# Performance work log

Hardware: AMD Instinct MI355X
Metric: run time of the kernel (lower is better)

The kernel has to match this reference:

```python
import jax, jax.numpy as jnp
import numpy as np

B, S, IN_DIM, MEM, LAYERS, HEADS, TOP_K = 64, 256, 512, 256, 3, 8, 200


def setup_inputs() -> dict:
    key = jax.random.key(0)
    ks = jax.random.split(key, 16)
    inputs = jax.random.normal(ks[0], (B, S, IN_DIM), jnp.float32)
    # dependency-style sparse 0/1 adjacency, symmetric with self loops
    a = (jax.random.uniform(ks[1], (B, S, S)) < 0.05).astype(jnp.float32)
    adj = jnp.clip(a + jnp.swapaxes(a, -1, -2) + jnp.eye(S, dtype=jnp.float32), 0.0, 1.0)
    lengths = jnp.maximum(jax.random.randint(ks[2], (B,), 0, S + 1), 32)
    pad = jnp.arange(S)[None, :] >= lengths[:, None]  # [B,S] True at pad positions
    score_mask = pad[:, None, :, None] | pad[:, None, None, :]  # [B,1,S,S]
    d = {"adj": adj, "inputs": inputs, "score_mask": score_mask}

    def lin(k, din, dout):
        k1, k2 = jax.random.split(k)
        s = 1.0 / np.sqrt(din)
        return (jax.random.uniform(k1, (din, dout), jnp.float32, -s, s),
                jax.random.uniform(k2, (dout,), jnp.float32, -s, s))

    ki = 3
    for l in range(LAYERS):
        w, b = lin(ks[ki], IN_DIM + l * MEM, MEM); ki += 1
        d[f"W{l}_w"], d[f"W{l}_b"] = w, b
    for i in range(LAYERS - 1):
        din = IN_DIM + (i + 1) * MEM
        qw, qb = lin(ks[ki], din, din); ki += 1
        kw, kb = lin(ks[ki], din, din); ki += 1
        d[f"attn{i}_qw"], d[f"attn{i}_qb"] = qw, qb
        d[f"attn{i}_kw"], d[f"attn{i}_kb"] = kw, kb
    return d


def _gcn_layer(adj, x, denom, W, b):
    # AxW = W(adj @ x) / denom ; out = relu(AxW) + W(x)   (dropout=identity, eval)
    AxW = ((adj @ x) @ W + b) / denom
    return jax.nn.relu(AxW) + (x @ W + b)


def _mha_adj(x, qw, qb, kw, kb, mask):
    Bn, Sn, D = x.shape
    dk = D // HEADS
    q = (x @ qw + qb).reshape(Bn, Sn, HEADS, dk).transpose(0, 2, 1, 3)
    k = (x @ kw + kb).reshape(Bn, Sn, HEADS, dk).transpose(0, 2, 1, 3)
    scores = jnp.einsum('bhqd,bhkd->bhqk', q, k) / jnp.sqrt(jnp.float32(dk))
    scores = jnp.where(mask, jnp.float32(-1e9), scores)
    keep = (~mask[:, :, :, 0:1]).astype(scores.dtype)  # zero out pad query rows
    return jax.nn.softmax(scores, axis=-1) * keep


def _select(m, top_num):
    # per-batch top-k threshold over flattened [S*S], symmetrize, diag := 1
    Bn, Sn, _ = m.shape
    flat = m.reshape(Bn, -1)
    thr = jax.lax.top_k(flat, top_num)[0][:, -1:]
    sel = (flat >= thr).astype(m.dtype).reshape(Bn, Sn, Sn)
    sel = sel + jnp.swapaxes(sel, -1, -2)
    eye = jnp.eye(Sn, dtype=m.dtype)
    return sel * (1.0 - eye) + eye


def reference(adj, inputs, score_mask, W0_w, W0_b, W1_w, W1_b, W2_w, W2_b,
              attn0_qw, attn0_qb, attn0_kw, attn0_kb,
              attn1_qw, attn1_qb, attn1_kw, attn1_kb):
    Ws = [(W0_w, W0_b), (W1_w, W1_b), (W2_w, W2_b)]
    attns = [(attn0_qw, attn0_qb, attn0_kw, attn0_kb),
             (attn1_qw, attn1_qb, attn1_kw, attn1_kb)]
    denom = adj.sum(2, keepdims=True) + 1.0
    out = _gcn_layer(adj, inputs, denom, *Ws[0])
    x = inputs
    for i in range(1, LAYERS):
        x = jnp.concatenate([x, out], axis=-1)  # growing concatenated features
        a = _mha_adj(x, *attns[i - 1], score_mask)  # [B,H,S,S]
        a = a.sum(axis=1)  # second_layer='sum' branch
        a = _select(a, TOP_K) * a
        denom = a.sum(2, keepdims=True) + 1.0
        out = _gcn_layer(a, x, denom, *Ws[i])
    return out
```

## Files before the change

kernel.cpp:

```cpp
#include <hip/hip_runtime.h>
#include <math.h>


typedef __attribute__((ext_vector_type(8))) short s16x8;
typedef __attribute__((ext_vector_type(4))) float f32x4;

__device__ __forceinline__ short f2bf(float x) {
    unsigned u = __float_as_uint(x);
    u += 0x7FFF + ((u >> 16) & 1);
    return (short)(u >> 16);
}
__device__ __forceinline__ float bf2f(short h) {
    return __uint_as_float(((unsigned)(unsigned short)h) << 16);
}

__device__ __forceinline__ void gl2l(const void* g, void* l) {
    __builtin_amdgcn_global_load_lds(
        (const __attribute__((address_space(1))) unsigned int*)g,
        (__attribute__((address_space(3))) unsigned int*)l, 16, 0, 0);
}

__global__ void init_flags(int* flags) {
    if (threadIdx.x < 3) flags[threadIdx.x] = 0;
}

__global__ void detect_mask(const unsigned int* __restrict__ w, int nwords, int* flags) {
    int stride = gridDim.x * blockDim.x;
    int l_u8 = 0, l_f32 = 0, l_nz = 0;
    for (int i = blockIdx.x * blockDim.x + threadIdx.x; i < nwords; i += stride) {
        unsigned v = w[i];
        if (v) {
            l_nz = 1;
            if (v == 0x3F800000u) l_f32 = 1;
            else if (v > 1u) l_u8 = 1;
        }
    }
    if (__ballot(l_u8) && (threadIdx.x & 63) == 0) atomicOr(&flags[0], 1);
    if (__ballot(l_f32) && (threadIdx.x & 63) == 0) atomicOr(&flags[1], 1);
    if (__ballot(l_nz) && (threadIdx.x & 63) == 0) atomicOr(&flags[2], 1);
}

__global__ void extract_pad(const void* __restrict__ mask, const int* __restrict__ flags,
                            unsigned char* __restrict__ pad) {
    int b = blockIdx.x, i = threadIdx.x;
    int v;
    size_t idx = (size_t)b * 65536 + (size_t)i * 256;
    if (flags[0]) v = ((const unsigned char*)mask)[idx] != 0;
    else if (flags[2]) v = ((const unsigned int*)mask)[idx] != 0;
    else v = 0;
    pad[b * 256 + i] = (unsigned char)v;
}

__global__ void build_live(const unsigned char* __restrict__ pad, int* __restrict__ live) {
    if (threadIdx.x == 0) {
        int c = 0;
        for (int t = 0; t < 128; ++t)
            if (!pad[t * 128]) live[1 + c++] = t;
        live[0] = c;
    }
}

__global__ void split_mat(const float* __restrict__ src, int ldsrc, int width,
                          short* __restrict__ dh, short* __restrict__ dl, int ldd) {
    int row = blockIdx.x;
    for (int c = threadIdx.x; c < width; c += 256) {
        float v = src[(size_t)row * ldsrc + c];
        short h = f2bf(v);
        dh[(size_t)row * ldd + c] = h;
        dl[(size_t)row * ldd + c] = f2bf(v - bf2f(h));
    }
}

__global__ void transpose_split(const float* __restrict__ in,
                                short* __restrict__ outh, short* __restrict__ outl,
                                int R, int C, int HR, long PSTR, int rowoff, int outld) {
    __shared__ float tile[32][33];
    int c0 = blockIdx.x * 32, r0 = blockIdx.y * 32;
    int tx = threadIdx.x & 31, ty = threadIdx.x >> 5;
    for (int rr = ty; rr < 32; rr += 8)
        tile[rr][tx] = in[(size_t)(r0 + rr) * C + c0 + tx];
    __syncthreads();
    for (int rr = ty; rr < 32; rr += 8) {
        float v = tile[tx][rr];
        int orow = c0 + rr;
        size_t o = (size_t)(orow / HR) * PSTR + (size_t)((orow % HR) + rowoff) * outld + (r0 + tx);
        short h = f2bf(v);
        outh[o] = h;
        outl[o] = f2bf(v - bf2f(h));
    }
}

__global__ void pack_bias2(const float* __restrict__ qb, const float* __restrict__ kb,
                           float* __restrict__ dst, int D) {
    int i = blockIdx.x * 256 + threadIdx.x;
    if (i < D) {
        int p = i / (D / 2), r = i % (D / 2);
        dst[(size_t)p * D + r] = qb[i];
        dst[(size_t)p * D + D / 2 + r] = kb[i];
    }
}

__global__ __launch_bounds__(256) void mgemm(
    const short* __restrict__ Ah, const short* __restrict__ Al,
    const short* __restrict__ Bh, const short* __restrict__ Bl,
    const float* __restrict__ bias,
    float* __restrict__ C, short* __restrict__ Ch, short* __restrict__ Cl,
    const unsigned char* __restrict__ padArr, const int* __restrict__ liveArr,
    int K, int lda, int ldb, int ldc, int coloff, int zdiv,
    long sA1, long sA2, long sB1, long sB2, long sC1, long sC2,
    float alpha, int skipmode, int swap) {
    int z = blockIdx.z, zq = z / zdiv, zr = z % zdiv;
    int m0, n0;
    if (swap) { m0 = blockIdx.x * 128; n0 = blockIdx.y * 128; }
    else      { m0 = blockIdx.y * 128; n0 = blockIdx.x * 128; }
    if (skipmode == 2 && (padArr[zr * 256 + m0] || padArr[zr * 256 + n0])) return;
    if (skipmode == 3) {
        int cnt = liveArr[0];
        if ((int)blockIdx.x >= cnt) return;
        m0 = liveArr[1 + blockIdx.x] * 128;
    }
    const short* Ahb = Ah + (size_t)zq * sA1 + (size_t)zr * sA2;
    const short* Alb = Al + (size_t)zq * sA1 + (size_t)zr * sA2;
    const short* Bhb = Bh + (size_t)zq * sB1 + (size_t)zr * sB2;
    const short* Blb = Bl + (size_t)zq * sB1 + (size_t)zr * sB2;
    size_t offC = (size_t)zq * sC1 + (size_t)zr * sC2;
    __shared__ short lds[16384];
    int t = threadIdx.x;
    int lane = t & 63, w = t >> 6;
    int wm = w >> 1, wn = w & 1;
    f32x4 acc[4][4];
#pragma unroll
    for (int i = 0; i < 4; ++i)
#pragma unroll
        for (int j = 0; j < 4; ++j)
            acc[i][j] = (f32x4){0.f, 0.f, 0.f, 0.f};

    for (int k0 = 0; k0 < K; k0 += 32) {
        __syncthreads();
#pragma unroll
        for (int p = 0; p < 2; ++p) {
            int s = t + p * 256;
            int mi = (s >> 6) * 16 + (s & 15);
            int koff = k0 + ((s >> 4) & 3) * 8;
            size_t oa = (size_t)(m0 + mi) * lda + koff;
            size_t ob = (size_t)(n0 + mi) * ldb + koff;
            gl2l(Ahb + oa, &lds[s * 8]);
            gl2l(Alb + oa, &lds[4096 + s * 8]);
            gl2l(Bhb + ob, &lds[8192 + s * 8]);
            gl2l(Blb + ob, &lds[12288 + s * 8]);
        }
        __syncthreads();
        s16x8 ah[4], al4[4], bh[4], bl4[4];
#pragma unroll
        for (int i = 0; i < 4; ++i) {
            int off = ((wm * 4 + i) * 64 + lane) * 8;
            ah[i] = *(const s16x8*)&lds[off];
            al4[i] = *(const s16x8*)&lds[4096 + off];
        }
#pragma unroll
        for (int j = 0; j < 4; ++j) {
            int off = ((wn * 4 + j) * 64 + lane) * 8;
            bh[j] = *(const s16x8*)&lds[8192 + off];
            bl4[j] = *(const s16x8*)&lds[12288 + off];
        }
#pragma unroll
        for (int i = 0; i < 4; ++i)
#pragma unroll
            for (int j = 0; j < 4; ++j) {
                acc[i][j] = __builtin_amdgcn_mfma_f32_16x16x32_bf16(ah[i], bh[j], acc[i][j], 0, 0, 0);
                acc[i][j] = __builtin_amdgcn_mfma_f32_16x16x32_bf16(ah[i], bl4[j], acc[i][j], 0, 0, 0);
                acc[i][j] = __builtin_amdgcn_mfma_f32_16x16x32_bf16(al4[i], bh[j], acc[i][j], 0, 0, 0);
            }
    }

    int col = lane & 15, quad = lane >> 4;
#pragma unroll
    for (int i = 0; i < 4; ++i)
#pragma unroll
        for (int j = 0; j < 4; ++j) {
            int mg = m0 + wm * 64 + i * 16 + quad * 4;
            int ng = n0 + wn * 64 + j * 16 + col;
            f32x4 v = acc[i][j];
            float bz = bias ? bias[ng] : 0.f;
            float o[4];
#pragma unroll
            for (int r = 0; r < 4; ++r) o[r] = v[r] * alpha + bz;
            if (C) {
                float* Cb = C + offC;
#pragma unroll
                for (int r = 0; r < 4; ++r)
                    Cb[(size_t)(mg + r) * ldc + coloff + ng] = o[r];
            }
            if (Ch) {
                short* Chb = Ch + offC;
                short* Clb = Cl + offC;
#pragma unroll
                for (int r = 0; r < 4; ++r) {
                    short hh = f2bf(o[r]);
                    Chb[(size_t)(mg + r) * ldc + coloff + ng] = hh;
                    Clb[(size_t)(mg + r) * ldc + coloff + ng] = f2bf(o[r] - bf2f(hh));
                }
            }
        }
}

__global__ void spmm_gcn(const float* __restrict__ A, const float* __restrict__ tz,
                         const float* __restrict__ bias,
                         short* __restrict__ oh, short* __restrict__ ol,
                         float* __restrict__ of, int ldo, int coloff) {
    int row = blockIdx.x * 4 + (threadIdx.x >> 6);
    int lane = threadIdx.x & 63;
    int b = row >> 8;
    float4 av = ((const float4*)(A + (size_t)row * 256))[lane];
    const float* tzb = tz + (size_t)(b << 8) * 256;
    float4 acc = make_float4(0.f, 0.f, 0.f, 0.f);
    float rs = av.x + av.y + av.z + av.w;
#pragma unroll
    for (int o = 32; o; o >>= 1) rs += __shfl_xor(rs, o);
    for (int s = 0; s < 64; ++s) {
        float vx = __shfl(av.x, s), vy = __shfl(av.y, s);
        float vz = __shfl(av.z, s), vw = __shfl(av.w, s);
        const float* tj = tzb + (size_t)(s << 2) * 256;
        if (vx != 0.f) {
            float4 tv = ((const float4*)tj)[lane];
            acc.x += vx * tv.x; acc.y += vx * tv.y; acc.z += vx * tv.z; acc.w += vx * tv.w;
        }
        if (vy != 0.f) {
            float4 tv = ((const float4*)(tj + 256))[lane];
            acc.x += vy * tv.x; acc.y += vy * tv.y; acc.z += vy * tv.z; acc.w += vy * tv.w;
        }
        if (vz != 0.f) {
            float4 tv = ((const float4*)(tj + 512))[lane];
            acc.x += vz * tv.x; acc.y += vz * tv.y; acc.z += vz * tv.z; acc.w += vz * tv.w;
        }
        if (vw != 0.f) {
            float4 tv = ((const float4*)(tj + 768))[lane];
            acc.x += vw * tv.x; acc.y += vw * tv.y; acc.z += vw * tv.z; acc.w += vw * tv.w;
        }
    }
    float inv = 1.f / (rs + 1.f);
    float4 b4 = ((const float4*)bias)[lane];
    float4 t4 = ((const float4*)(tz + (size_t)row * 256))[lane];
    float4 o;
    o.x = fmaxf((acc.x + b4.x) * inv, 0.f) + t4.x + b4.x;
    o.y = fmaxf((acc.y + b4.y) * inv, 0.f) + t4.y + b4.y;
    o.z = fmaxf((acc.z + b4.z) * inv, 0.f) + t4.z + b4.z;
    o.w = fmaxf((acc.w + b4.w) * inv, 0.f) + t4.w + b4.w;
    if (of) {
        ((float4*)(of + (size_t)row * ldo))[lane] = o;
    } else {
        size_t base = (size_t)row * ldo + coloff + lane * 4;
        float vv[4] = {o.x, o.y, o.z, o.w};
#pragma unroll
        for (int r = 0; r < 4; ++r) {
            short hh = f2bf(vv[r]);
            oh[base + r] = hh;
            ol[base + r] = f2bf(vv[r] - bf2f(hh));
        }
    }
}

__global__ void softmax_headsum2(const float* __restrict__ scores,
                                 const unsigned char* __restrict__ pad,
                                 float* __restrict__ a, int accum) {
    int row = blockIdx.x * 4 + (threadIdx.x >> 6);
    int lane = threadIdx.x & 63;
    int b = row >> 8;
    float* arow = a + (size_t)row * 256;
    if (pad[row]) {
        if (!accum) ((float4*)arow)[lane] = make_float4(0.f, 0.f, 0.f, 0.f);
        return;
    }
    unsigned pw = *(const unsigned*)(pad + (b << 8) + lane * 4);
    float4 racc;
    if (accum) racc = ((float4*)arow)[lane];
    else racc = make_float4(0.f, 0.f, 0.f, 0.f);
#pragma unroll
    for (int hh = 0; hh < 2; ++hh) {
        float4 s = ((const float4*)(scores + (size_t)hh * 4194304 + (size_t)row * 256))[lane];
        if (pw & 0x000000FFu) s.x = -1e9f;
        if (pw & 0x0000FF00u) s.y = -1e9f;
        if (pw & 0x00FF0000u) s.z = -1e9f;
        if (pw & 0xFF000000u) s.w = -1e9f;
        float m = fmaxf(fmaxf(s.x, s.y), fmaxf(s.z, s.w));
#pragma unroll
        for (int o = 32; o; o >>= 1) m = fmaxf(m, __shfl_xor(m, o));
        float e0 = expf(s.x - m), e1 = expf(s.y - m), e2 = expf(s.z - m), e3 = expf(s.w - m);
        float sum = e0 + e1 + e2 + e3;
#pragma unroll
        for (int o = 32; o; o >>= 1) sum += __shfl_xor(sum, o);
        float inv = 1.f / sum;
        racc.x += e0 * inv; racc.y += e1 * inv; racc.z += e2 * inv; racc.w += e3 * inv;
    }
    ((float4*)arow)[lane] = racc;
}

__global__ void tk_init(unsigned* ghist, unsigned* prefix, int* krem) {
    int i = blockIdx.x * 256 + threadIdx.x;
    ghist[i] = 0;
    if (i < 64) { prefix[i] = 0; krem[i] = 200; }
}

__global__ void tk_hist(const float* __restrict__ a, const unsigned* __restrict__ prefix,
                        unsigned* __restrict__ ghist, int shift) {
    __shared__ unsigned h[256];
    int b = blockIdx.x >> 4, slice = blockIdx.x & 15;
    h[threadIdx.x] = 0;
    __syncthreads();
    unsigned pfx = prefix[b];
    const unsigned* ab = (const unsigned*)(a + (size_t)b * 65536) + slice * 4096;
    for (int i = threadIdx.x; i < 4096; i += 256) {
        unsigned u = ab[i];
        if ((shift == 24) || ((u >> (shift + 8)) == pfx)) atomicAdd(&h[(u >> shift) & 255], 1u);
    }
    __syncthreads();
    if (h[threadIdx.x]) atomicAdd(&ghist[b * 256 + threadIdx.x], h[threadIdx.x]);
}

__global__ void tk_pick(unsigned* __restrict__ ghist, unsigned* __restrict__ prefix,
                        int* __restrict__ krem, float* __restrict__ thr, int last) {
    __shared__ unsigned h[256];
    int b = blockIdx.x;
    h[threadIdx.x] = ghist[b * 256 + threadIdx.x];
    ghist[b * 256 + threadIdx.x] = 0;
    __syncthreads();
    if (!threadIdx.x) {
        int k = krem[b];
        unsigned c = 0;
        int bin = 255;
        for (; bin >= 0; --bin) { c += h[bin]; if ((int)c >= k) break; }
        if (bin < 0) bin = 0;
        krem[b] = k - (int)(c - h[bin]);
        unsigned p = (prefix[b] << 8) | (unsigned)bin;
        prefix[b] = p;
        if (last) thr[b] = __uint_as_float(p);
    }
}

__global__ void select_apply(const float* __restrict__ a, const float* __restrict__ thr,
                             float* __restrict__ a2) {
    int row = blockIdx.x;
    int b = row >> 8, i = row & 255, j = threadIdx.x;
    const float* ab = a + (size_t)b * 65536;
    float tb = thr[b];
    float v = ab[i * 256 + j];
    float vt = ab[j * 256 + i];
    float sel = (v >= tb ? 1.f : 0.f) + (vt >= tb ? 1.f : 0.f);
    if (i == j) sel = 1.f;
    a2[(size_t)row * 256 + j] = v * sel;
}

extern "C" void kernel_launch(void* const* d_in, const int* in_sizes, int n_in,
                              void* d_out, int out_size, void* d_ws, size_t ws_size,
                              hipStream_t stream) {
    const float* adj = (const float*)d_in[0];
    const float* x0 = (const float*)d_in[1];
    const void* mask = d_in[2];
    const float* Wls[3] = {(const float*)d_in[3], (const float*)d_in[5], (const float*)d_in[7]};
    const float* bls[3] = {(const float*)d_in[4], (const float*)d_in[6], (const float*)d_in[8]};
    const float* qws[2] = {(const float*)d_in[9], (const float*)d_in[13]};
    const float* qbs[2] = {(const float*)d_in[10], (const float*)d_in[14]};
    const float* kws[2] = {(const float*)d_in[11], (const float*)d_in[15]};
    const float* kbs[2] = {(const float*)d_in[12], (const float*)d_in[16]};

    char* base = (char*)d_ws;
    size_t cur = 0;
    auto alloc = [&](size_t bytes) -> void* {
        cur = (cur + 1023) & ~(size_t)1023;
        void* p = base + cur;
        cur += bytes;
        return p;
    };
    const size_t NROW = 16384;
    int* flags = (int*)alloc(12);
    unsigned char* pad = (unsigned char*)alloc(NROW);
    float* thr = (float*)alloc(256);
    unsigned* prefix = (unsigned*)alloc(256);
    int* krem = (int*)alloc(256);
    int* live = (int*)alloc(516);
    unsigned* ghist = (unsigned*)alloc(64 * 256 * 4);
    short* WTh = (short*)alloc((size_t)2304 * 256 * 2);
    short* WTl = (short*)alloc((size_t)2304 * 256 * 2);
    short* qkwPh = (short*)alloc((size_t)2 * 1024 * 1024 * 2);
    short* qkwPl = (short*)alloc((size_t)2 * 1024 * 1024 * 2);
    float* qkb = (float*)alloc((size_t)2 * 1024 * 4);
    short* xh = (short*)alloc(NROW * 1024 * 2);
    short* xl = (short*)alloc(NROW * 1024 * 2);
    float* tzf = (float*)alloc(NROW * 256 * 4);
    float* scores = (float*)alloc((size_t)2 * 64 * 65536 * 4);
    float* a = (float*)alloc(NROW * 256 * 4);
    float* a2f = (float*)alloc(NROW * 256 * 4);
    short* QKh = (short*)alloc(NROW * 1024 * 2);
    short* QKl = (short*)alloc(NROW * 1024 * 2);
    if (ws_size < cur) return;

    const int Ks[3] = {512, 768, 1024};
    const long offW[3] = {0, (long)512 * 256, (long)(512 + 768) * 256};

    init_flags<<<1, 64, 0, stream>>>(flags);
    detect_mask<<<64, 256, 0, stream>>>((const unsigned int*)mask, 1048576, flags);
    extract_pad<<<64, 256, 0, stream>>>(mask, flags, pad);
    build_live<<<1, 64, 0, stream>>>(pad, live);
    split_mat<<<16384, 256, 0, stream>>>(x0, 512, 512, xh, xl, 1024);
    for (int l = 0; l < 3; ++l)
        transpose_split<<<dim3(8, Ks[l] / 32), 256, 0, stream>>>(
            Wls[l], WTh + offW[l], WTl + offW[l], Ks[l], 256, 256, 0, 0, Ks[l]);

    for (int l = 0; l < 3; ++l) {
        int Kl = Ks[l];
        mgemm<<<dim3(128, 2, 1), 256, 0, stream>>>(
            xh, xl, WTh + offW[l], WTl + offW[l], nullptr,
            tzf, nullptr, nullptr, nullptr, nullptr,
            Kl, 1024, Kl, 256, 0, 1,
            0, 0, 0, 0, 0, 0, 1.f, 0, 1);
        const float* Aadj = (l == 0) ? adj : a2f;
        if (l < 2) {
            spmm_gcn<<<4096, 256, 0, stream>>>(
                Aadj, tzf, bls[l], xh, xl, nullptr, 1024, Kl);
        } else {
            spmm_gcn<<<4096, 256, 0, stream>>>(
                Aadj, tzf, bls[l], nullptr, nullptr, (float*)d_out, 256, 0);
            break;
        }

        int D = Ks[l + 1], dk = D / 8, HD = D / 2;
        float scale = 1.f / sqrtf((float)dk);
        transpose_split<<<dim3(D / 32, D / 32), 256, 0, stream>>>(
            qws[l], qkwPh, qkwPl, D, D, HD, (long)D * D, 0, D);
        transpose_split<<<dim3(D / 32, D / 32), 256, 0, stream>>>(
            kws[l], qkwPh, qkwPl, D, D, HD, (long)D * D, HD, D);
        pack_bias2<<<4, 256, 0, stream>>>(qbs[l], kbs[l], qkb, D);

        for (int p = 0; p < 2; ++p) {
            mgemm<<<dim3(128, D / 128, 1), 256, 0, stream>>>(
                xh, xl, qkwPh + (size_t)p * D * D, qkwPl + (size_t)p * D * D, qkb + (size_t)p * D,
                nullptr, QKh, QKl, nullptr, live,
                D, 1024, D, D, 0, 1,
                0, 0, 0, 0, 0, 0, 1.f, 3, 1);
            for (int hp = 0; hp < 2; ++hp) {
                mgemm<<<dim3(2, 2, 128), 256, 0, stream>>>(
                    QKh + (size_t)(hp * 2) * dk, QKl + (size_t)(hp * 2) * dk,
                    QKh + HD + (size_t)(hp * 2) * dk, QKl + HD + (size_t)(hp * 2) * dk,
                    nullptr, scores, nullptr, nullptr, pad, nullptr,
                    dk, D, D, 256, 0, 64,
                    dk, (long)256 * D, dk, (long)256 * D, (long)64 * 65536, 65536,
                    scale, 2, 0);
                softmax_headsum2<<<4096, 256, 0, stream>>>(scores, pad, a, (p * 2 + hp) ? 1 : 0);
            }
        }
        tk_init<<<64, 256, 0, stream>>>(ghist, prefix, krem);
        for (int pp = 0; pp < 4; ++pp) {
            tk_hist<<<1024, 256, 0, stream>>>(a, prefix, ghist, 24 - 8 * pp);
            tk_pick<<<64, 256, 0, stream>>>(ghist, prefix, krem, thr, pp == 3);
        }
        select_apply<<<16384, 256, 0, stream>>>(a, thr, a2f);
    }
}
```

Baseline: 1.469 ms.

## Fuse per-head QK scores, masked softmax and head-sum into one attention kernel

Replaces the batched score GEMM, the scores buffer and the separate softmax/head-sum kernel with one kernel. It computes Q·Kᵀ for two heads per block with the split-bf16 MFMA scheme, then does masked softmax in registers with cross-wave LDS reductions and accumulates the head sum. The four partial head-sum slices are written out and combined by a small add4 kernel. The generic mgemm is simplified: the live-tile list and strided batching are dropped and padded row tiles are skipped directly from the pad array. Workspace buffers are aliased onto the new partial-sum buffer. This removes the large fp32 score round trip and several launches, but adds extra partial-sum traffic and higher register pressure in the fused kernel.

```diff
diff --git a/kernel.cpp b/kernel.cpp
--- a/kernel.cpp
+++ b/kernel.cpp
@@ -49,15 +49,6 @@
     else if (flags[2]) v = ((const unsigned int*)mask)[idx] != 0;
     else v = 0;
     pad[b * 256 + i] = (unsigned char)v;
-}
-
-__global__ void build_live(const unsigned char* __restrict__ pad, int* __restrict__ live) {
-    if (threadIdx.x == 0) {
-        int c = 0;
-        for (int t = 0; t < 128; ++t)
-            if (!pad[t * 128]) live[1 + c++] = t;
-        live[0] = c;
-    }
 }
 
 __global__ void split_mat(const float* __restrict__ src, int ldsrc, int width,
@@ -105,25 +96,10 @@
     const short* __restrict__ Bh, const short* __restrict__ Bl,
     const float* __restrict__ bias,
     float* __restrict__ C, short* __restrict__ Ch, short* __restrict__ Cl,
-    const unsigned char* __restrict__ padArr, const int* __restrict__ liveArr,
-    int K, int lda, int ldb, int ldc, int coloff, int zdiv,
-    long sA1, long sA2, long sB1, long sB2, long sC1, long sC2,
-    float alpha, int skipmode, int swap) {
-    int z = blockIdx.z, zq = z / zdiv, zr = z % zdiv;
-    int m0, n0;
-    if (swap) { m0 = blockIdx.x * 128; n0 = blockIdx.y * 128; }
-    else      { m0 = blockIdx.y * 128; n0 = blockIdx.x * 128; }
-    if (skipmode == 2 && (padArr[zr * 256 + m0] || padArr[zr * 256 + n0])) return;
-    if (skipmode == 3) {
-        int cnt = liveArr[0];
-        if ((int)blockIdx.x >= cnt) return;
-        m0 = liveArr[1 + blockIdx.x] * 128;
-    }
-    const short* Ahb = Ah + (size_t)zq * sA1 + (size_t)zr * sA2;
-    const short* Alb = Al + (size_t)zq * sA1 + (size_t)zr * sA2;
-    const short* Bhb = Bh + (size_t)zq * sB1 + (size_t)zr * sB2;
-    const short* Blb = Bl + (size_t)zq * sB1 + (size_t)zr * sB2;
-    size_t offC = (size_t)zq * sC1 + (size_t)zr * sC2;
+    const unsigned char* __restrict__ padArr,
+    int K, int lda, int ldb, int ldc) {
+    int m0 = blockIdx.x * 128, n0 = blockIdx.y * 128;
+    if (padArr && padArr[m0]) return;
     __shared__ short lds[16384];
     int t = threadIdx.x;
     int lane = t & 63, w = t >> 6;
@@ -144,10 +120,10 @@
             int koff = k0 + ((s >> 4) & 3) * 8;
             size_t oa = (size_t)(m0 + mi) * lda + koff;
             size_t ob = (size_t)(n0 + mi) * ldb + koff;
-            gl2l(Ahb + oa, &lds[s * 8]);
-            gl2l(Alb + oa, &lds[4096 + s * 8]);
-            gl2l(Bhb + ob, &lds[8192 + s * 8]);
-            gl2l(Blb + ob, &lds[12288 + s * 8]);
+            gl2l(Ah + oa, &lds[s * 8]);
+            gl2l(Al + oa, &lds[4096 + s * 8]);
+            gl2l(Bh + ob, &lds[8192 + s * 8]);
+            gl2l(Bl + ob, &lds[12288 + s * 8]);
         }
         __syncthreads();
         s16x8 ah[4], al4[4], bh[4], bl4[4];
@@ -184,21 +160,17 @@
             float bz = bias ? bias[ng] : 0.f;
             float o[4];
 #pragma unroll
-            for (int r = 0; r < 4; ++r) o[r] = v[r] * alpha + bz;
+            for (int r = 0; r < 4; ++r) o[r] = v[r] + bz;
             if (C) {
-                float* Cb = C + offC;
 #pragma unroll
                 for (int r = 0; r < 4; ++r)
-                    Cb[(size_t)(mg + r) * ldc + coloff + ng] = o[r];
-            }
-            if (Ch) {
-                short* Chb = Ch + offC;
-                short* Clb = Cl + offC;
+                    C[(size_t)(mg + r) * ldc + ng] = o[r];
+            } else {
 #pragma unroll
                 for (int r = 0; r < 4; ++r) {
                     short hh = f2bf(o[r]);
-                    Chb[(size_t)(mg + r) * ldc + coloff + ng] = hh;
-                    Clb[(size_t)(mg + r) * ldc + coloff + ng] = f2bf(o[r] - bf2f(hh));
+                    Ch[(size_t)(mg + r) * ldc + ng] = hh;
+                    Cl[(size_t)(mg + r) * ldc + ng] = f2bf(o[r] - bf2f(hh));
                 }
             }
         }
@@ -260,39 +232,189 @@
     }
 }
 
-__global__ void softmax_headsum2(const float* __restrict__ scores,
-                                 const unsigned char* __restrict__ pad,
-                                 float* __restrict__ a, int accum) {
+__global__ __launch_bounds__(256) void attn_fused(
+    const short* __restrict__ QKh, const short* __restrict__ QKl,
+    const unsigned char* __restrict__ pad, float* __restrict__ a4,
+    int D, int dk, float scale) {
+    int HD = D / 2;
+    int b = blockIdx.y;
+    int m0 = blockIdx.x * 64;
+    const unsigned char* pb = pad + (b << 8);
+    if (pb[m0]) return;
+    int t = threadIdx.x, lane = t & 63, w = t >> 6;
+    int wm = w >> 1, wn = w & 1;
+    int col16 = lane & 15, quad = lane >> 4;
+    __shared__ short lds[20480];
+    __shared__ float redm[64][2];
+    __shared__ float reds[64][2];
+    unsigned cmask = 0;
+#pragma unroll
+    for (int j = 0; j < 8; ++j)
+        if (pb[wn * 128 + j * 16 + col16]) cmask |= 1u << j;
+    float* a4b = a4 + (size_t)blockIdx.z * 4194304;
+    size_t rowQ = (size_t)(b << 8) + m0;
+    size_t rowK = (size_t)(b << 8);
+    float aacc[2][8][4];
+#pragma unroll
+    for (int i = 0; i < 2; ++i)
+#pragma unroll
+        for (int j = 0; j < 8; ++j)
+#pragma unroll
+            for (int r = 0; r < 4; ++r) aacc[i][j][r] = 0.f;
+
+    for (int hh = 0; hh < 2; ++hh) {
+        int hs = blockIdx.z * 2 + hh;
+        int qo = hs * dk, ko = HD + hs * dk;
+        f32x4 acc[2][8];
+#pragma unroll
+        for (int i = 0; i < 2; ++i)
+#pragma unroll
+            for (int j = 0; j < 8; ++j) acc[i][j] = (f32x4){0.f, 0.f, 0.f, 0.f};
+        for (int k0 = 0; k0 < dk; k0 += 32) {
+            __syncthreads();
+            {
+                int mi = ((t >> 6) << 4) + (t & 15);
+                int kc = ((t >> 4) & 3) << 3;
+                size_t o = (rowQ + mi) * D + qo + k0 + kc;
+                gl2l(QKh + o, &lds[t * 8]);
+                gl2l(QKl + o, &lds[2048 + t * 8]);
+            }
+#pragma unroll
+            for (int kk = 0; kk < 4; ++kk) {
+                int s = t + (kk << 8);
+                int ni = ((s >> 6) << 4) + (s & 15);
+                int kc = ((s >> 4) & 3) << 3;
+                size_t o = (rowK + ni) * D + ko + k0 + kc;
+                gl2l(QKh + o, &lds[4096 + s * 8]);
+                gl2l(QKl + o, &lds[12288 + s * 8]);
+            }
+            __syncthreads();
+            s16x8 qh[2], ql[2];
+#pragma unroll
+            for (int i = 0; i < 2; ++i) {
+                int off = ((wm * 2 + i) * 64 + lane) * 8;
+                qh[i] = *(const s16x8*)&lds[off];
+                ql[i] = *(const s16x8*)&lds[2048 + off];
+            }
+#pragma unroll
+            for (int j = 0; j < 8; ++j) {
+                int off = ((wn * 8 + j) * 64 + lane) * 8;
+                s16x8 kh = *(const s16x8*)&lds[4096 + off];
+                s16x8 kl = *(const s16x8*)&lds[12288 + off];
+#pragma unroll
+                for (int i = 0; i < 2; ++i) {
+                    acc[i][j] = __builtin_amdgcn_mfma_f32_16x16x32_bf16(qh[i], kh, acc[i][j], 0, 0, 0);
+                    acc[i][j] = __builtin_amdgcn_mfma_f32_16x16x32_bf16(qh[i], kl, acc[i][j], 0, 0, 0);
+                    acc[i][j] = __builtin_amdgcn_mfma_f32_16x16x32_bf16(ql[i], kh, acc[i][j], 0, 0, 0);
+                }
+            }
+        }
+        float rmax[2][4];
+#pragma unroll
+        for (int i = 0; i < 2; ++i)
+#pragma unroll
+            for (int r = 0; r < 4; ++r) rmax[i][r] = -1e30f;
+#pragma unroll
+        for (int i = 0; i < 2; ++i)
+#pragma unroll
+            for (int j = 0; j < 8; ++j) {
+                bool msk = (cmask >> j) & 1;
+#pragma unroll
+                for (int r = 0; r < 4; ++r) {
+                    float v = msk ? -1e30f : acc[i][j][r] * scale;
+                    acc[i][j][r] = v;
+                    rmax[i][r] = fmaxf(rmax[i][r], v);
+                }
+            }
+#pragma unroll
+        for (int ms = 1; ms < 16; ms <<= 1)
+#pragma unroll
+            for (int i = 0; i < 2; ++i)
+#pragma unroll
+                for (int r = 0; r < 4; ++r)
+                    rmax[i][r] = fmaxf(rmax[i][r], __shfl_xor(rmax[i][r], ms));
+        if (col16 == 0)
+#pragma unroll
+            for (int i = 0; i < 2; ++i)
+#pragma unroll
+                for (int r = 0; r < 4; ++r)
+                    redm[wm * 32 + i * 16 + quad * 4 + r][wn] = rmax[i][r];
+        __syncthreads();
+#pragma unroll
+        for (int i = 0; i < 2; ++i)
+#pragma unroll
+            for (int r = 0; r < 4; ++r) {
+                int rr = wm * 32 + i * 16 + quad * 4 + r;
+                rmax[i][r] = fmaxf(redm[rr][0], redm[rr][1]);
+            }
+        float rsum[2][4];
+#pragma unroll
+        for (int i = 0; i < 2; ++i)
+#pragma unroll
+            for (int r = 0; r < 4; ++r) rsum[i][r] = 0.f;
+#pragma unroll
+        for (int i = 0; i < 2; ++i)
+#pragma unroll
+            for (int j = 0; j < 8; ++j) {
+                bool msk = (cmask >> j) & 1;
+#pragma unroll
+                for (int r = 0; r < 4; ++r) {
+                    float p = msk ? 0.f : __expf(acc[i][j][r] - rmax[i][r]);
+                    acc[i][j][r] = p;
+                    rsum[i][r] += p;
+                }
+            }
+#pragma unroll
+        for (int ms = 1; ms < 16; ms <<= 1)
+#pragma unroll
+            for (int i = 0; i < 2; ++i)
+#pragma unroll
+                for (int r = 0; r < 4; ++r)
+                    rsum[i][r] += __shfl_xor(rsum[i][r], ms);
+        if (col16 == 0)
+#pragma unroll
+            for (int i = 0; i < 2; ++i)
+#pragma unroll
+                for (int r = 0; r < 4; ++r)
+                    reds[wm * 32 + i * 16 + quad * 4 + r][wn] = rsum[i][r];
+        __syncthreads();
+#pragma unroll
+        for (int i = 0; i < 2; ++i)
+#pragma unroll
+            for (int r = 0; r < 4; ++r) {
+                int rr = wm * 32 + i * 16 + quad * 4 + r;
+                float tot = reds[rr][0] + reds[rr][1];
+                float inv = tot > 0.f ? 1.f / tot : 0.f;
+#pragma unroll
+                for (int j = 0; j < 8; ++j)
+                    aacc[i][j][r] += acc[i][j][r] * inv;
+            }
+    }
+#pragma unroll
+    for (int i = 0; i < 2; ++i)
+#pragma unroll
+        for (int r = 0; r < 4; ++r) {
+            size_t rb = (rowQ + wm * 32 + i * 16 + quad * 4 + r) * 256;
+#pragma unroll
+            for (int j = 0; j < 8; ++j)
+                a4b[rb + wn * 128 + j * 16 + col16] = aacc[i][j][r];
+        }
+}
+
+__global__ void add4(const float* __restrict__ a4, const unsigned char* __restrict__ pad,
+                     float* __restrict__ a) {
     int row = blockIdx.x * 4 + (threadIdx.x >> 6);
     int lane = threadIdx.x & 63;
-    int b = row >> 8;
-    float* arow = a + (size_t)row * 256;
-    if (pad[row]) {
-        if (!accum) ((float4*)arow)[lane] = make_float4(0.f, 0.f, 0.f, 0.f);
-        return;
-    }
-    unsigned pw = *(const unsigned*)(pad + (b << 8) + lane * 4);
-    float4 racc;
-    if (accum) racc = ((float4*)arow)[lane];
-    else racc = make_float4(0.f, 0.f, 0.f, 0.f);
-#pragma unroll
-    for (int hh = 0; hh < 2; ++hh) {
-        float4 s = ((const float4*)(scores + (size_t)hh * 4194304 + (size_t)row * 256))[lane];
-        if (pw & 0x000000FFu) s.x = -1e9f;
-        if (pw & 0x0000FF00u) s.y = -1e9f;
-        if (pw & 0x00FF0000u) s.z = -1e9f;
-        if (pw & 0xFF000000u) s.w = -1e9f;
-        float m = fmaxf(fmaxf(s.x, s.y), fmaxf(s.z, s.w));
-#pragma unroll
-        for (int o = 32; o; o >>= 1) m = fmaxf(m, __shfl_xor(m, o));
-        float e0 = expf(s.x - m), e1 = expf(s.y - m), e2 = expf(s.z - m), e3 = expf(s.w - m);
-        float sum = e0 + e1 + e2 + e3;
-#pragma unroll
-        for (int o = 32; o; o >>= 1) sum += __shfl_xor(sum, o);
-        float inv = 1.f / sum;
-        racc.x += e0 * inv; racc.y += e1 * inv; racc.z += e2 * inv; racc.w += e3 * inv;
-    }
-    ((float4*)arow)[lane] = racc;
+    size_t o = (size_t)row * 256 + lane * 4;
+    float4 s = make_float4(0.f, 0.f, 0.f, 0.f);
+    if (!pad[row]) {
+#pragma unroll
+        for (int z = 0; z < 4; ++z) {
+            float4 v = *(const float4*)(a4 + (size_t)z * 4194304 + o);
+            s.x += v.x; s.y += v.y; s.z += v.z; s.w += v.w;
+        }
+    }
+    *(float4*)(a + o) = s;
 }
 
 __global__ void tk_init(unsigned* ghist, unsigned* prefix, int* krem) {
@@ -372,12 +494,12 @@
         return p;
     };
     const size_t NROW = 16384;
+    const size_t SEG = NROW * 256;
     int* flags = (int*)alloc(12);
     unsigned char* pad = (unsigned char*)alloc(NROW);
     float* thr = (float*)alloc(256);
     unsigned* prefix = (unsigned*)alloc(256);
     int* krem = (int*)alloc(256);
-    int* live = (int*)alloc(516);
     unsigned* ghist = (unsigned*)alloc(64 * 256 * 4);
     short* WTh = (short*)alloc((size_t)2304 * 256 * 2);
     short* WTl = (short*)alloc((size_t)2304 * 256 * 2);
@@ -386,21 +508,20 @@
     float* qkb = (float*)alloc((size_t)2 * 1024 * 4);
     short* xh = (short*)alloc(NROW * 1024 * 2);
     short* xl = (short*)alloc(NROW * 1024 * 2);
-    float* tzf = (float*)alloc(NROW * 256 * 4);
-    float* scores = (float*)alloc((size_t)2 * 64 * 65536 * 4);
-    float* a = (float*)alloc(NROW * 256 * 4);
-    float* a2f = (float*)alloc(NROW * 256 * 4);
+    float* a4 = (float*)alloc(4 * SEG * 4);
     short* QKh = (short*)alloc(NROW * 1024 * 2);
     short* QKl = (short*)alloc(NROW * 1024 * 2);
     if (ws_size < cur) return;
 
+    float* a = a4;
+    float* tzf = a4 + SEG;
+    float* a2f = a4 + 3 * SEG;
     const int Ks[3] = {512, 768, 1024};
     const long offW[3] = {0, (long)512 * 256, (long)(512 + 768) * 256};
 
     init_flags<<<1, 64, 0, stream>>>(flags);
     detect_mask<<<64, 256, 0, stream>>>((const unsigned int*)mask, 1048576, flags);
     extract_pad<<<64, 256, 0, stream>>>(mask, flags, pad);
-    build_live<<<1, 64, 0, stream>>>(pad, live);
     split_mat<<<16384, 256, 0, stream>>>(x0, 512, 512, xh, xl, 1024);
     for (int l = 0; l < 3; ++l)
         transpose_split<<<dim3(8, Ks[l] / 32), 256, 0, stream>>>(
@@ -410,9 +531,7 @@
         int Kl = Ks[l];
         mgemm<<<dim3(128, 2, 1), 256, 0, stream>>>(
             xh, xl, WTh + offW[l], WTl + offW[l], nullptr,
-            tzf, nullptr, nullptr, nullptr, nullptr,
-            Kl, 1024, Kl, 256, 0, 1,
-            0, 0, 0, 0, 0, 0, 1.f, 0, 1);
+            tzf, nullptr, nullptr, nullptr, Kl, 1024, Kl, 256);
         const float* Aadj = (l == 0) ? adj : a2f;
         if (l < 2) {
             spmm_gcn<<<4096, 256, 0, stream>>>(
@@ -433,21 +552,12 @@
 
         for (int p = 0; p < 2; ++p) {
             mgemm<<<dim3(128, D / 128, 1), 256, 0, stream>>>(
-                xh, xl, qkwPh + (size_t)p * D * D, qkwPl + (size_t)p * D * D, qkb + (size_t)p * D,
-                nullptr, QKh, QKl, nullptr, live,
-                D, 1024, D, D, 0, 1,
-                0, 0, 0, 0, 0, 0, 1.f, 3, 1);
-            for (int hp = 0; hp < 2; ++hp) {
-                mgemm<<<dim3(2, 2, 128), 256, 0, stream>>>(
-                    QKh + (size_t)(hp * 2) * dk, QKl + (size_t)(hp * 2) * dk,
-                    QKh + HD + (size_t)(hp * 2) * dk, QKl + HD + (size_t)(hp * 2) * dk,
-                    nullptr, scores, nullptr, nullptr, pad, nullptr,
-                    dk, D, D, 256, 0, 64,
-                    dk, (long)256 * D, dk, (long)256 * D, (long)64 * 65536, 65536,
-                    scale, 2, 0);
-                softmax_headsum2<<<4096, 256, 0, stream>>>(scores, pad, a, (p * 2 + hp) ? 1 : 0);
-            }
-        }
+                xh, xl, qkwPh + (size_t)p * D * D, qkwPl + (size_t)p * D * D,
+                qkb + (size_t)p * D, nullptr, QKh, QKl, pad, D, 1024, D, D);
+            attn_fused<<<dim3(4, 64, 2), 256, 0, stream>>>(
+                QKh, QKl, pad, a4 + (size_t)p * 2 * SEG, D, dk, scale);
+        }
+        add4<<<4096, 256, 0, stream>>>(a4, pad, a);
         tk_init<<<64, 256, 0, stream>>>(ghist, prefix, krem);
         for (int pp = 0; pp < 4; ++pp) {
             tk_hist<<<1024, 256, 0, stream>>>(a, prefix, ghist, 24 - 8 * pp);
```

Result: faster. 1.384 ms (-5.8%).
